# Optimization experiments

Hardware: AMD Instinct MI355X
Metric: run time of the kernel (lower is better)

## Reference

```python
import jax, jax.numpy as jnp
import numpy as np

B, T, D, H = 2, 2048, 1024, 16
HD = D // H
DFF = 4 * D
EPS = 1e-5


def gelu_tanh(x):
    c = jnp.sqrt(2.0 / jnp.pi).astype(x.dtype)
    return 0.5 * x * (1.0 + jnp.tanh(c * (x + 0.044715 * x ** 3)))


def layernorm(x, scale, shift):
    mean = jnp.mean(x, axis=-1, keepdims=True)
    var = jnp.var(x, axis=-1, keepdims=True)  # unbiased=False
    return (x - mean) / jnp.sqrt(var + EPS) * scale + shift


def setup_inputs() -> dict:
    key = jax.random.key(0)
    ks = jax.random.split(key, 12)
    s = lambda fan_in: 1.0 / np.sqrt(fan_in)
    return {
        "x": jax.random.normal(ks[0], (B, T, D), jnp.float32),
        "wq": jax.random.normal(ks[1], (D, D), jnp.float32) * s(D),
        "wk": jax.random.normal(ks[2], (D, D), jnp.float32) * s(D),
        "wv": jax.random.normal(ks[3], (D, D), jnp.float32) * s(D),
        "wo": jax.random.normal(ks[4], (D, D), jnp.float32) * s(D),
        "bo": jnp.zeros((D,), jnp.float32),
        "ln1_scale": jnp.ones((D,), jnp.float32),
        "ln1_shift": jnp.zeros((D,), jnp.float32),
        "ln2_scale": jnp.ones((D,), jnp.float32),
        "ln2_shift": jnp.zeros((D,), jnp.float32),
        "w1": jax.random.normal(ks[5], (D, DFF), jnp.float32) * s(D),
        "b1": jnp.zeros((DFF,), jnp.float32),
        "w2": jax.random.normal(ks[6], (DFF, D), jnp.float32) * s(DFF),
        "b2": jnp.zeros((D,), jnp.float32),
    }


def reference(x, wq, wk, wv, wo, bo, ln1_scale, ln1_shift, ln2_scale, ln2_shift, w1, b1, w2, b2):
    # pre-LN attention
    h = layernorm(x, ln1_scale, ln1_shift)
    q = (h @ wq).reshape(B, T, H, HD).transpose(0, 2, 1, 3)  # [B,H,T,hd]
    k = (h @ wk).reshape(B, T, H, HD).transpose(0, 2, 1, 3)
    v = (h @ wv).reshape(B, T, H, HD).transpose(0, 2, 1, 3)
    scores = jnp.einsum('bhqd,bhkd->bhqk', q, k) / jnp.sqrt(jnp.float32(HD))
    causal = jnp.tril(jnp.ones((T, T), bool))
    scores = jnp.where(causal, scores, -jnp.inf)
    attn = jax.nn.softmax(scores, axis=-1)
    ctx = jnp.einsum('bhqk,bhkd->bhqd', attn, v)
    ctx = ctx.transpose(0, 2, 1, 3).reshape(B, T, D)
    attn_out = ctx @ wo + bo
    x = x + attn_out  # dropout p=0
    # pre-LN FFN
    h2 = layernorm(x, ln2_scale, ln2_shift)
    ff = gelu_tanh(h2 @ w1 + b1) @ w2 + b2
    return x + ff
```

## Files before the change

### kernel.cpp

```cpp
#include <hip/hip_runtime.h>
#include <hip/hip_bf16.h>
#include <stdint.h>

typedef unsigned short u16;
typedef __attribute__((ext_vector_type(8))) short s16x8;
typedef __attribute__((ext_vector_type(4))) float f32x4;

#define B_   2
#define T_   2048
#define D_   1024
#define H_   16
#define HD_  64
#define DFF_ 4096
#define M_   (B_*T_)

#define SC2F 0.18033688f

__device__ __forceinline__ u16 f2b(float f){
  uint32_t u = __float_as_uint(f);
  u += 0x7FFFu + ((u >> 16) & 1u);
  return (u16)(u >> 16);
}
__device__ __forceinline__ float b2f(u16 u){ return __uint_as_float(((uint32_t)u) << 16); }
__device__ __forceinline__ uint32_t pk2(float lo, float hi){
  uint32_t r;
  asm volatile("v_cvt_pk_bf16_f32 %0, %1, %2" : "=v"(r) : "v"(lo), "v"(hi));
  return r;
}

__device__ __forceinline__ void gl_lds16(const void* g, void* l){
  __builtin_amdgcn_global_load_lds((const __attribute__((address_space(1))) void*)g,
                                   (__attribute__((address_space(3))) void*)l, 16, 0, 0);
}

template<int N> __device__ __forceinline__ void waitvm(){
  if constexpr (N == 0)      asm volatile("s_waitcnt vmcnt(0)" ::: "memory");
  else if constexpr (N == 2) asm volatile("s_waitcnt vmcnt(2)" ::: "memory");
  else                       asm volatile("s_waitcnt vmcnt(4)" ::: "memory");
}

__global__ __launch_bounds__(256) void wconv_all(const float* __restrict__ wq,
                                                 const float* __restrict__ wk,
                                                 const float* __restrict__ wv,
                                                 const float* __restrict__ wo,
                                                 const float* __restrict__ w1,
                                                 const float* __restrict__ w2,
                                                 u16* __restrict__ wqkvT, u16* __restrict__ woT,
                                                 u16* __restrict__ w1T,   u16* __restrict__ w2T,
                                                 const float* __restrict__ x,
                                                 const float* __restrict__ ln1s,
                                                 const float* __restrict__ ln1b,
                                                 u16* __restrict__ hout){
  const int bid = blockIdx.x;
  const int tid = threadIdx.x;
  if (bid >= 3072){
    const int row = bid - 3072;
    float4 a = reinterpret_cast<const float4*>(x + ((size_t)row << 10))[tid];
    float s = a.x + a.y + a.z + a.w;
    float q = a.x*a.x + a.y*a.y + a.z*a.z + a.w*a.w;
    #pragma unroll
    for (int o = 32; o > 0; o >>= 1){ s += __shfl_xor(s, o); q += __shfl_xor(q, o); }
    __shared__ float red[8];
    const int w = tid >> 6;
    if ((tid & 63) == 0){ red[w] = s; red[4 + w] = q; }
    __syncthreads();
    float S = red[0] + red[1] + red[2] + red[3];
    float Q = red[4] + red[5] + red[6] + red[7];
    float mean = S * (1.0f/1024.0f);
    float var  = Q * (1.0f/1024.0f) - mean*mean;
    float inv = rsqrtf(var + 1e-5f);
    float4 gsc = reinterpret_cast<const float4*>(ln1s)[tid];
    float4 gsh = reinterpret_cast<const float4*>(ln1b)[tid];
    ushort4 o4;
    o4.x = f2b((a.x - mean)*inv*gsc.x + gsh.x);
    o4.y = f2b((a.y - mean)*inv*gsc.y + gsh.y);
    o4.z = f2b((a.z - mean)*inv*gsc.z + gsh.z);
    o4.w = f2b((a.w - mean)*inv*gsc.w + gsh.w);
    reinterpret_cast<ushort4*>(hout + ((size_t)row << 10))[tid] = o4;
    return;
  }
  const float* W; u16* Wt; int K, N, tk, tn;
  if (bid < 1024){
    const int which = bid >> 8, t = bid & 255; tk = t >> 4; tn = t & 15; K = 1024; N = 1024;
    W  = (which == 0) ? wq : (which == 1) ? wk : (which == 2) ? wv : wo;
    Wt = (which == 3) ? woT : wqkvT + (size_t)which * D_ * D_;
  } else if (bid < 2048){
    const int t = bid - 1024; tk = t >> 6; tn = t & 63; K = 1024; N = 4096; W = w1; Wt = w1T;
  } else {
    const int t = bid - 2048; tk = t >> 4; tn = t & 15; K = 4096; N = 1024; W = w2; Wt = w2T;
  }
  const int k0 = tk << 6, n0 = tn << 6;
  __shared__ u16 tile[64][68];
  const int rr = tid >> 4, c4 = (tid & 15) << 2;
  #pragma unroll
  for (int rep = 0; rep < 4; rep++){
    int r = rr + (rep << 4);
    float4 v = *reinterpret_cast<const float4*>(W + (size_t)(k0 + r)*N + n0 + c4);
    tile[r][c4+0] = f2b(v.x); tile[r][c4+1] = f2b(v.y);
    tile[r][c4+2] = f2b(v.z); tile[r][c4+3] = f2b(v.w);
  }
  __syncthreads();
  const int rn = tid >> 2, kb = (tid & 3) << 4;
  u16 tmp[16];
  #pragma unroll
  for (int j = 0; j < 16; j++) tmp[j] = tile[kb + j][rn];
  ushort4* dst = reinterpret_cast<ushort4*>(Wt + (size_t)(n0 + rn)*K + k0 + kb);
  dst[0] = make_ushort4(tmp[0], tmp[1], tmp[2], tmp[3]);
  dst[1] = make_ushort4(tmp[4], tmp[5], tmp[6], tmp[7]);
  dst[2] = make_ushort4(tmp[8], tmp[9], tmp[10], tmp[11]);
  dst[3] = make_ushort4(tmp[12], tmp[13], tmp[14], tmp[15]);
}

__global__ __launch_bounds__(256) void vtrans(const u16* __restrict__ Vs, u16* __restrict__ Vt){
  const int bh = blockIdx.y, tt = blockIdx.x;
  __shared__ u16 tile[64][68];
  const int tid = threadIdx.x;
  const u16* src = Vs + ((size_t)bh*T_ + tt*64)*HD_;
  const int rr = tid >> 4, c4 = (tid & 15) << 2;
  #pragma unroll
  for (int rep = 0; rep < 4; rep++){
    int r = rr + (rep << 4);
    ushort4 v = *reinterpret_cast<const ushort4*>(src + (size_t)r*HD_ + c4);
    tile[r][c4+0] = v.x; tile[r][c4+1] = v.y; tile[r][c4+2] = v.z; tile[r][c4+3] = v.w;
  }
  __syncthreads();
  const int rn = tid >> 2, kb = (tid & 3) << 4;
  u16 tmp[16];
  #pragma unroll
  for (int j = 0; j < 16; j++) tmp[j] = tile[kb + j][rn];
  ushort4* dst = reinterpret_cast<ushort4*>(Vt + ((size_t)bh*HD_ + rn)*T_ + tt*64 + kb);
  dst[0] = make_ushort4(tmp[0], tmp[1], tmp[2], tmp[3]);
  dst[1] = make_ushort4(tmp[4], tmp[5], tmp[6], tmp[7]);
  dst[2] = make_ushort4(tmp[8], tmp[9], tmp[10], tmp[11]);
  dst[3] = make_ushort4(tmp[12], tmp[13], tmp[14], tmp[15]);
}

__global__ __launch_bounds__(256) void reduce2(const u16* __restrict__ p,
                                               const float* __restrict__ bias,
                                               const float* __restrict__ resid,
                                               float* __restrict__ out){
  const size_t idx = ((size_t)blockIdx.x << 8) + threadIdx.x;
  ushort4 a4 = reinterpret_cast<const ushort4*>(p)[idx];
  ushort4 b4 = reinterpret_cast<const ushort4*>(p)[idx + (((size_t)M_*D_) >> 2)];
  float4 r = reinterpret_cast<const float4*>(resid)[idx];
  float4 bb = reinterpret_cast<const float4*>(bias)[threadIdx.x];
  float4 o;
  o.x = b2f(a4.x) + b2f(b4.x) + r.x + bb.x;
  o.y = b2f(a4.y) + b2f(b4.y) + r.y + bb.y;
  o.z = b2f(a4.z) + b2f(b4.z) + r.z + bb.z;
  o.w = b2f(a4.w) + b2f(b4.w) + r.w + bb.w;
  reinterpret_cast<float4*>(out)[idx] = o;
}

__global__ __launch_bounds__(256) void reduce_ln(const u16* __restrict__ p,
                                                 const float* __restrict__ bias,
                                                 const float* __restrict__ resid,
                                                 const float* __restrict__ sc,
                                                 const float* __restrict__ sh,
                                                 float* __restrict__ x1,
                                                 u16* __restrict__ h2){
  const int row = blockIdx.x;
  const int tid = threadIdx.x;
  const size_t idx = ((size_t)row << 8) + tid;
  ushort4 a4 = reinterpret_cast<const ushort4*>(p)[idx];
  ushort4 b4 = reinterpret_cast<const ushort4*>(p)[idx + (((size_t)M_*D_) >> 2)];
  float4 r  = reinterpret_cast<const float4*>(resid)[idx];
  float4 bb = reinterpret_cast<const float4*>(bias)[tid];
  float4 v;
  v.x = b2f(a4.x) + b2f(b4.x) + r.x + bb.x;
  v.y = b2f(a4.y) + b2f(b4.y) + r.y + bb.y;
  v.z = b2f(a4.z) + b2f(b4.z) + r.z + bb.z;
  v.w = b2f(a4.w) + b2f(b4.w) + r.w + bb.w;
  reinterpret_cast<float4*>(x1)[idx] = v;
  float s = v.x + v.y + v.z + v.w;
  float q = v.x*v.x + v.y*v.y + v.z*v.z + v.w*v.w;
  #pragma unroll
  for (int o = 32; o > 0; o >>= 1){ s += __shfl_xor(s, o); q += __shfl_xor(q, o); }
  __shared__ float red[8];
  const int w = tid >> 6;
  if ((tid & 63) == 0){ red[w] = s; red[4 + w] = q; }
  __syncthreads();
  float S = red[0] + red[1] + red[2] + red[3];
  float Q = red[4] + red[5] + red[6] + red[7];
  float mean = S * (1.0f/1024.0f);
  float var  = Q * (1.0f/1024.0f) - mean*mean;
  float inv = rsqrtf(var + 1e-5f);
  float4 gsc = reinterpret_cast<const float4*>(sc)[tid];
  float4 gsh = reinterpret_cast<const float4*>(sh)[tid];
  ushort4 o4;
  o4.x = f2b((v.x - mean)*inv*gsc.x + gsh.x);
  o4.y = f2b((v.y - mean)*inv*gsc.y + gsh.y);
  o4.z = f2b((v.z - mean)*inv*gsc.z + gsh.z);
  o4.w = f2b((v.w - mean)*inv*gsc.w + gsh.w);
  reinterpret_cast<ushort4*>(h2 + ((size_t)row << 10))[tid] = o4;
}

template<int EPI, int NF>
__global__ __launch_bounds__(512, 2) void gemm8(const u16* __restrict__ A, const u16* __restrict__ Bt,
                                                const float* __restrict__ bias,
                                                void* __restrict__ Cv, int M, int N, int K, int lda){
  constexpr int BROWS = NF * 32;
  __shared__ __align__(16) u16 LA[2][2][128*64];
  __shared__ __align__(16) u16 LB[2][2][BROWS*64];
  const int tid = threadIdx.x;
  const int lane = tid & 63;
  const int w = tid >> 6;
  const int wm = w >> 2, wn = w & 3;
  const int g = lane >> 4, l15 = lane & 15;
  const int bnb = (wn & 1) * (NF * 16);

  const int nx = gridDim.x, ny = gridDim.y;
  const int nwg = nx * ny * gridDim.z;
  const int flat = blockIdx.x + nx * (blockIdx.y + ny * blockIdx.z);
  const int nfid = (flat & 7) * (nwg >> 3) + (flat >> 3);
  const int tn = nfid % nx;
  const int rest = nfid / nx;
  const int tm = rest % ny;
  const int kz = rest / ny;
  const int tn0 = tn * (NF * 64);
  const int tm0 = tm << 8;
  const u16* Az = A  + (size_t)kz * K;
  const u16* Bz = Bt + (size_t)kz * K;

  const int arow0 = tid >> 3,         asl0 = (((tid) & 7) ^ (arow0 & 7)) << 3;
  const int arow1 = (tid + 512) >> 3, asl1 = (((tid + 512) & 7) ^ (arow1 & 7)) << 3;

  f32x4 acc[8][NF];
  #pragma unroll
  for (int i = 0; i < 8; i++)
    #pragma unroll
    for (int j = 0; j < NF; j++) acc[i][j] = (f32x4){0.f,0.f,0.f,0.f};
  s16x8 bf[NF][2];

#define STG_A(db, h, tt) do{                                                        \
    gl_lds16(Az + (size_t)(tm0 + (h)*128 + arow0)*lda + ((tt) << 6) + asl0,         \
             &LA[db][h][tid*8]);                                                    \
    gl_lds16(Az + (size_t)(tm0 + (h)*128 + arow1)*lda + ((tt) << 6) + asl1,         \
             &LA[db][h][(tid + 512)*8]);                                            \
  }while(0)
#define STG_B(db, h, tt) do{                                                        \
    gl_lds16(Bz + (size_t)(tn0 + (h)*BROWS + arow0)*lda + ((tt) << 6) + asl0,       \
             &LB[db][h][tid*8]);                                                    \
    if constexpr (NF == 4){                                                         \
      gl_lds16(Bz + (size_t)(tn0 + (h)*BROWS + arow1)*lda + ((tt) << 6) + asl1,     \
               &LB[db][h][(tid + 512)*8]);                                          \
    }                                                                               \
  }while(0)
#define LDAF(db, mf, kk) (*reinterpret_cast<const s16x8*>(                          \
    &LA[db][wm][((mf)*16 + l15)*64 + ((((kk)*4 + g) ^ (l15 & 7)) << 3)]))
#define LDBF(db, nf, kk) (*reinterpret_cast<const s16x8*>(                          \
    &LB[db][wn >> 1][(bnb + (nf)*16 + l15)*64 + ((((kk)*4 + g) ^ (l15 & 7)) << 3)]))
#define BLOAD(db) do{ _Pragma("unroll")                                             \
    for (int nf = 0; nf < NF; nf++){ bf[nf][0] = LDBF(db, nf, 0);                   \
                                     bf[nf][1] = LDBF(db, nf, 1); } }while(0)
#define PH(db, MFA, MFB, STG, WV) do{                                               \
    s16x8 a00 = LDAF(db, MFA, 0), a01 = LDAF(db, MFA, 1);                           \
    s16x8 a10 = LDAF(db, MFB, 0), a11 = LDAF(db, MFB, 1);                           \
    STG;                                                                            \
    WV;                                                                             \
    __builtin_amdgcn_s_barrier();                                                   \
    __builtin_amdgcn_s_setprio(1);                                                  \
    _Pragma("unroll")                                                               \
    for (int nf = 0; nf < NF; nf++){                                                \
      acc[MFA][nf] = __builtin_amdgcn_mfma_f32_16x16x32_bf16(a00, bf[nf][0], acc[MFA][nf], 0,0,0); \
      acc[MFA][nf] = __builtin_amdgcn_mfma_f32_16x16x32_bf16(a01, bf[nf][1], acc[MFA][nf], 0,0,0); \
      acc[MFB][nf] = __builtin_amdgcn_mfma_f32_16x16x32_bf16(a10, bf[nf][0], acc[MFB][nf], 0,0,0); \
      acc[MFB][nf] = __builtin_amdgcn_mfma_f32_16x16x32_bf16(a11, bf[nf][1], acc[MFB][nf], 0,0,0); \
    }                                                                               \
    __builtin_amdgcn_s_setprio(0);                                                  \
    __builtin_amdgcn_s_barrier();                                                   \
  }while(0)

  const int NT = K >> 6;
  STG_B(0, 0, 0); STG_B(0, 1, 0); STG_A(0, 0, 0); STG_A(0, 1, 0);
  STG_B(1, 0, 1); STG_B(1, 1, 1);
  waitvm<NF>();
  __builtin_amdgcn_s_barrier();

  for (int t = 0; t < NT; t += 2){
    const bool last = (t + 2 >= NT);
    BLOAD(0);
    PH(0, 0, 1, STG_A(1, 0, t + 1), );
    PH(0, 2, 3, STG_A(1, 1, t + 1), );
    PH(0, 4, 5, if (!last) STG_B(0, 0, t + 2), );
    PH(0, 6, 7, if (!last) STG_B(0, 1, t + 2),
                if (last) waitvm<0>(); else waitvm<NF>(););
    BLOAD(1);
    PH(1, 0, 1, if (!last) STG_A(0, 0, t + 2), );
    PH(1, 2, 3, if (!last) STG_A(0, 1, t + 2), );
    PH(1, 4, 5, if (!last) STG_B(1, 0, t + 3), );
    PH(1, 6, 7, if (!last) STG_B(1, 1, t + 3),
                if (last) waitvm<0>(); else waitvm<NF>(););
  }
#undef STG_A
#undef STG_B
#undef LDAF
#undef LDBF
#undef BLOAD
#undef PH

  #pragma unroll
  for (int mf = 0; mf < 8; mf++){
    const int mb = tm0 + wm*128 + mf*16 + (g << 2);
    #pragma unroll
    for (int nf = 0; nf < NF; nf++){
      const int n = tn0 + wn*(NF*16) + nf*16 + l15;
      #pragma unroll
      for (int rr = 0; rr < 4; rr++){
        const int m = mb + rr;
        float v = acc[mf][nf][rr];
        if constexpr (EPI == 0){
          ((u16*)Cv)[(size_t)kz*((size_t)M*N) + (size_t)m*N + n] = f2b(v);
        } else if constexpr (EPI == 1){
          const int sel = n >> 10, nn = n & 1023;
          const int hh = nn >> 6, d = nn & 63;
          if (sel == 0) v *= SC2F;
          ((u16*)Cv)[(size_t)sel*((size_t)M_*D_) +
                     ((((size_t)(m >> 11)*H_ + hh)*T_ + (m & 2047)) << 6) + d] = f2b(v);
        } else {
          float u = v + bias[n];
          float t2 = 0.7978845608f*(u + 0.044715f*u*u*u);
          float e = __expf(2.0f*t2);
          float th = 1.0f - 2.0f/(e + 1.0f);
          ((u16*)Cv)[(size_t)m*N + n] = f2b(0.5f*u*(1.0f + th));
        }
      }
    }
  }
}

__global__ __launch_bounds__(512) void attn_k(const u16* __restrict__ Qg, const u16* __restrict__ Kg,
                                              const u16* __restrict__ Vg, u16* __restrict__ ctx){
  const int flat = blockIdx.x + (blockIdx.y << 4);
  const int xcd = flat & 7;
  const int j_  = (flat >> 3) & 31;
  const int half = flat >> 8;
  const int bh  = ((j_ & 3) << 3) + xcd;
  const int pr_ = j_ >> 2;
  const int qt  = half ? (15 - pr_) : pr_;
  const int NKT = (qt << 1) + 2;
  const int tid = threadIdx.x;
  const int lane = tid & 63;
  const int w = tid >> 6;
  const int g = lane >> 4, l15 = lane & 15;

  __shared__ __align__(16) u16 Qs[128*64];
  __shared__ __align__(16) u16 Ks[2][64*64];
  __shared__ __align__(16) u16 Vt[2][64*64];
  __shared__ __align__(16) u16 Pl[8][16*64];

  const size_t hb = (size_t)bh * ((size_t)T_*HD_);
  const u16* Qh = Qg + hb;
  const u16* Kh = Kg + hb;
  const u16* Vh = Vg + hb;
  const int b = bh >> 4, hh = bh & 15;

  const int s_r0 = tid >> 3,         s_c0 = (((tid & 7) ^ (s_r0 & 7)) << 3);
  const int s_r1 = (tid + 512) >> 3, s_c1 = ((((tid + 512) & 7) ^ (s_r1 & 7)) << 3);

  gl_lds16(Qh + (size_t)(qt*128 + s_r0)*HD_ + s_c0, Qs + tid*8);
  gl_lds16(Qh + (size_t)(qt*128 + s_r1)*HD_ + s_c1, Qs + (tid+512)*8);
  gl_lds16(Kh + (size_t)s_r0*HD_ + s_c0, Ks[0] + tid*8);
  gl_lds16(Vh + (size_t)s_r0*T_ + s_c0, Vt[0] + tid*8);
  __syncthreads();

  s16x8 qa[2];
  #pragma unroll
  for (int kk = 0; kk < 2; kk++){
    int ra = (w << 4) + l15;
    int slot = (kk << 2) + g;
    qa[kk] = *reinterpret_cast<const s16x8*>(Qs + ra*64 + ((slot ^ (ra & 7)) << 3));
  }

  f32x4 accO[4];
  #pragma unroll
  for (int j = 0; j < 4; j++) accO[j] = (f32x4){0.f,0.f,0.f,0.f};
  float mrow = -1e30f, lrow = 0.f;
  const int qgl = qt*128 + (w << 4) + l15;

  for (int kt = 0; kt < NKT; ++kt){
    const int cur = kt & 1, nxt = cur ^ 1;
    const bool pf = (kt + 1 < NKT);

    if (pf){
      gl_lds16(Kh + (size_t)((kt+1)*64 + s_r0)*HD_ + s_c0, Ks[nxt] + tid*8);
      gl_lds16(Vh + (size_t)s_r0*T_ + (kt+1)*64 + s_c0, Vt[nxt] + tid*8);
    }

    f32x4 accS[4];
    #pragma unroll
    for (int j = 0; j < 4; j++) accS[j] = (f32x4){0.f,0.f,0.f,0.f};
    __builtin_amdgcn_s_setprio(1);
    #pragma unroll
    for (int jn = 0; jn < 4; jn++){
      #pragma unroll
      for (int kk = 0; kk < 2; kk++){
        int rb = (jn << 4) + l15;
        int slot = (kk << 2) + g;
        s16x8 kf = *reinterpret_cast<const s16x8*>(Ks[cur] + rb*64 + ((slot ^ (rb & 7)) << 3));
        accS[jn] = __builtin_amdgcn_mfma_f32_16x16x32_bf16(kf, qa[kk], accS[jn], 0, 0, 0);
      }
    }
    __builtin_amdgcn_s_setprio(0);

    if (kt >= (qt << 1)){
      #pragma unroll
      for (int jn = 0; jn < 4; jn++)
        #pragma unroll
        for (int rr = 0; rr < 4; rr++){
          int kgl = kt*64 + (jn << 4) + (g << 2) + rr;
          if (kgl > qgl) accS[jn][rr] = -1e30f;
        }
    }

    float rmax = accS[0][0];
    #pragma unroll
    for (int jn = 0; jn < 4; jn++)
      #pragma unroll
      for (int rr = 0; rr < 4; rr++) rmax = fmaxf(rmax, accS[jn][rr]);
    rmax = fmaxf(rmax, __shfl_xor(rmax, 16));
    rmax = fmaxf(rmax, __shfl_xor(rmax, 32));

    if (__any(rmax > mrow + 8.0f)){
      float mn = fmaxf(mrow, rmax);
      float sf = exp2f(mrow - mn);
      mrow = mn;
      lrow *= sf;
      #pragma unroll
      for (int rr = 0; rr < 4; rr++){
        float sfr = __shfl(sf, ((lane >> 4) << 2) + rr);
        #pragma unroll
        for (int jn = 0; jn < 4; jn++) accO[jn][rr] *= sfr;
      }
    }

    float tsum = 0.f;
    #pragma unroll
    for (int jn = 0; jn < 4; jn++){
      float pv0 = exp2f(accS[jn][0] - mrow);
      float pv1 = exp2f(accS[jn][1] - mrow);
      float pv2 = exp2f(accS[jn][2] - mrow);
      float pv3 = exp2f(accS[jn][3] - mrow);
      tsum += (pv0 + pv1) + (pv2 + pv3);
      int slot = (jn << 1) | (g >> 1);
      int base = l15*64 + (((slot ^ (l15 & 7)) & 7) << 3) + ((g & 1) << 2);
      uint2 pkd = make_uint2(pk2(pv0, pv1), pk2(pv2, pv3));
      *reinterpret_cast<uint2*>(&Pl[w][base]) = pkd;
    }
    tsum += __shfl_xor(tsum, 16);
    tsum += __shfl_xor(tsum, 32);
    lrow += tsum;

    __builtin_amdgcn_s_setprio(1);
    #pragma unroll
    for (int kk = 0; kk < 2; kk++){
      int slot = (kk << 2) + g;
      s16x8 pa = *reinterpret_cast<const s16x8*>(
          &Pl[w][l15*64 + (((slot ^ (l15 & 7)) & 7) << 3)]);
      #pragma unroll
      for (int jn = 0; jn < 4; jn++){
        int vd = (jn << 4) + l15;
        s16x8 vbf = *reinterpret_cast<const s16x8*>(
            Vt[cur] + vd*64 + (((slot ^ (vd & 7)) & 7) << 3));
        accO[jn] = __builtin_amdgcn_mfma_f32_16x16x32_bf16(pa, vbf, accO[jn], 0, 0, 0);
      }
    }
    __builtin_amdgcn_s_setprio(0);

    __syncthreads();
  }

  #pragma unroll
  for (int rr = 0; rr < 4; rr++){
    float lr = __shfl(lrow, ((lane >> 4) << 2) + rr);
    float inv = 1.0f / lr;
    int qrow = qt*128 + (w << 4) + (g << 2) + rr;
    size_t rowbase = ((size_t)(b*T_ + qrow) << 10) + ((size_t)hh << 6);
    #pragma unroll
    for (int jn = 0; jn < 4; jn++){
      int d = (jn << 4) + l15;
      ctx[rowbase + d] = f2b(accO[jn][rr] * inv);
    }
  }
}

extern "C" void kernel_launch(void* const* d_in, const int* in_sizes, int n_in,
                              void* d_out, int out_size, void* d_ws, size_t ws_size,
                              hipStream_t stream){
  (void)in_sizes; (void)n_in; (void)out_size; (void)ws_size;
  const float* x    = (const float*)d_in[0];
  const float* wq   = (const float*)d_in[1];
  const float* wk   = (const float*)d_in[2];
  const float* wv   = (const float*)d_in[3];
  const float* wo   = (const float*)d_in[4];
  const float* bo   = (const float*)d_in[5];
  const float* ln1s = (const float*)d_in[6];
  const float* ln1b = (const float*)d_in[7];
  const float* ln2s = (const float*)d_in[8];
  const float* ln2b = (const float*)d_in[9];
  const float* w1   = (const float*)d_in[10];
  const float* b1   = (const float*)d_in[11];
  const float* w2   = (const float*)d_in[12];
  const float* b2   = (const float*)d_in[13];
  float* out = (float*)d_out;

  char* p = (char*)d_ws;
  u16*  wqkvT = (u16*)p;  p += (size_t)3*D_*D_*2;
  u16*  woT   = (u16*)p;  p += (size_t)D_*D_*2;
  u16*  w1T   = (u16*)p;  p += (size_t)D_*DFF_*2;
  u16*  w2T   = (u16*)p;  p += (size_t)DFF_*D_*2;
  u16*  h     = (u16*)p;  p += (size_t)M_*D_*2;
  u16*  qb    = (u16*)p;  p += (size_t)M_*D_*2;
  u16*  kb    = (u16*)p;  p += (size_t)M_*D_*2;
  u16*  vb    = (u16*)p;  p += (size_t)M_*D_*2;
  u16*  ctx   = (u16*)p;  p += (size_t)M_*D_*2;
  float* x1   = (float*)p; p += (size_t)M_*D_*4;
  u16*  h2    = (u16*)p;  p += (size_t)M_*D_*2;
  u16*  ff1   = (u16*)p;  p += (size_t)M_*DFF_*2;
  (void)kb;
  u16* part = h;

  dim3 blk(256), blk8(512);
  wconv_all<<<3072 + M_, blk, 0, stream>>>(wq, wk, wv, wo, w1, w2, wqkvT, woT, w1T, w2T,
                                           x, ln1s, ln1b, h);
  gemm8<1,4><<<dim3(12,16,1), blk8, 0, stream>>>(h, wqkvT, nullptr, qb, M_, 3*D_, D_, D_);
  vtrans<<<dim3(32,32), blk, 0, stream>>>(vb, h);
  attn_k<<<dim3(16,32), blk8, 0, stream>>>(qb, qb + (size_t)M_*D_, h, ctx);
  gemm8<0,2><<<dim3(8,16,2), blk8, 0, stream>>>(ctx, woT, nullptr, part, M_, D_, D_/2, D_);
  reduce_ln<<<M_, blk, 0, stream>>>(part, bo, x, ln2s, ln2b, x1, h2);
  gemm8<3,4><<<dim3(16,16,1), blk8, 0, stream>>>(h2, w1T, b1, ff1, M_, DFF_, D_, D_);
  gemm8<0,2><<<dim3(8,16,2), blk8, 0, stream>>>(ff1, w2T, nullptr, part, M_, D_, DFF_/2, DFF_);
  reduce2<<<M_, blk, 0, stream>>>(part, b2, x1, out);
}
```

Measured before the change: 231.4 us.

## Fuse V transpose into QKV GEMM epilogue and reuse Q smem for P

The QKV GEMM epilogue now writes the V block directly in transposed [b,h,d,t] layout through an LDS staging tile, so the separate vtrans kernel and its round trip through global memory are gone. The attention kernel drops its dedicated P buffer and reuses each wave's slice of the Q shared tile, which lowers LDS use and may allow higher occupancy. It also changes the block-to-(head, q-tile) mapping so adjacent blocks pair light and heavy causal tiles. The cost is extra syncs in the V-epilogue tiles, and the P-in-Q reuse is only safe if Q fragments are fully held in registers first.

Result: no change. 230.9 us (-0.2%).

```diff
diff --git a/kernel.cpp b/kernel.cpp
--- a/kernel.cpp
+++ b/kernel.cpp
@@ -105,30 +105,6 @@
   #pragma unroll
   for (int j = 0; j < 16; j++) tmp[j] = tile[kb + j][rn];
   ushort4* dst = reinterpret_cast<ushort4*>(Wt + (size_t)(n0 + rn)*K + k0 + kb);
-  dst[0] = make_ushort4(tmp[0], tmp[1], tmp[2], tmp[3]);
-  dst[1] = make_ushort4(tmp[4], tmp[5], tmp[6], tmp[7]);
-  dst[2] = make_ushort4(tmp[8], tmp[9], tmp[10], tmp[11]);
-  dst[3] = make_ushort4(tmp[12], tmp[13], tmp[14], tmp[15]);
-}
-
-__global__ __launch_bounds__(256) void vtrans(const u16* __restrict__ Vs, u16* __restrict__ Vt){
-  const int bh = blockIdx.y, tt = blockIdx.x;
-  __shared__ u16 tile[64][68];
-  const int tid = threadIdx.x;
-  const u16* src = Vs + ((size_t)bh*T_ + tt*64)*HD_;
-  const int rr = tid >> 4, c4 = (tid & 15) << 2;
-  #pragma unroll
-  for (int rep = 0; rep < 4; rep++){
-    int r = rr + (rep << 4);
-    ushort4 v = *reinterpret_cast<const ushort4*>(src + (size_t)r*HD_ + c4);
-    tile[r][c4+0] = v.x; tile[r][c4+1] = v.y; tile[r][c4+2] = v.z; tile[r][c4+3] = v.w;
-  }
-  __syncthreads();
-  const int rn = tid >> 2, kb = (tid & 3) << 4;
-  u16 tmp[16];
-  #pragma unroll
-  for (int j = 0; j < 16; j++) tmp[j] = tile[kb + j][rn];
-  ushort4* dst = reinterpret_cast<ushort4*>(Vt + ((size_t)bh*HD_ + rn)*T_ + tt*64 + kb);
   dst[0] = make_ushort4(tmp[0], tmp[1], tmp[2], tmp[3]);
   dst[1] = make_ushort4(tmp[4], tmp[5], tmp[6], tmp[7]);
   dst[2] = make_ushort4(tmp[8], tmp[9], tmp[10], tmp[11]);
@@ -198,7 +174,8 @@
 template<int EPI, int NF>
 __global__ __launch_bounds__(512, 2) void gemm8(const u16* __restrict__ A, const u16* __restrict__ Bt,
                                                 const float* __restrict__ bias,
-                                                void* __restrict__ Cv, int M, int N, int K, int lda){
+                                                void* __restrict__ Cv, void* __restrict__ Cv2,
+                                                int M, int N, int K, int lda){
   constexpr int BROWS = NF * 32;
   __shared__ __align__(16) u16 LA[2][2][128*64];
   __shared__ __align__(16) u16 LB[2][2][BROWS*64];
@@ -299,30 +276,86 @@
 #undef BLOAD
 #undef PH
 
-  #pragma unroll
-  for (int mf = 0; mf < 8; mf++){
-    const int mb = tm0 + wm*128 + mf*16 + (g << 2);
-    #pragma unroll
-    for (int nf = 0; nf < NF; nf++){
-      const int n = tn0 + wn*(NF*16) + nf*16 + l15;
-      #pragma unroll
-      for (int rr = 0; rr < 4; rr++){
-        const int m = mb + rr;
-        float v = acc[mf][nf][rr];
-        if constexpr (EPI == 0){
-          ((u16*)Cv)[(size_t)kz*((size_t)M*N) + (size_t)m*N + n] = f2b(v);
-        } else if constexpr (EPI == 1){
-          const int sel = n >> 10, nn = n & 1023;
+  if constexpr (EPI == 1){
+    const int sel = tn0 >> 10;
+    if (sel < 2){
+      #pragma unroll
+      for (int mf = 0; mf < 8; mf++){
+        const int mb = tm0 + wm*128 + mf*16 + (g << 2);
+        #pragma unroll
+        for (int nf = 0; nf < NF; nf++){
+          const int n = tn0 + wn*(NF*16) + nf*16 + l15;
+          const int nn = n & 1023;
           const int hh = nn >> 6, d = nn & 63;
-          if (sel == 0) v *= SC2F;
-          ((u16*)Cv)[(size_t)sel*((size_t)M_*D_) +
-                     ((((size_t)(m >> 11)*H_ + hh)*T_ + (m & 2047)) << 6) + d] = f2b(v);
-        } else {
-          float u = v + bias[n];
-          float t2 = 0.7978845608f*(u + 0.044715f*u*u*u);
-          float e = __expf(2.0f*t2);
-          float th = 1.0f - 2.0f/(e + 1.0f);
-          ((u16*)Cv)[(size_t)m*N + n] = f2b(0.5f*u*(1.0f + th));
+          #pragma unroll
+          for (int rr = 0; rr < 4; rr++){
+            const int m = mb + rr;
+            float v = acc[mf][nf][rr];
+            if (sel == 0) v *= SC2F;
+            ((u16*)Cv)[(size_t)sel*((size_t)M_*D_) +
+                       ((((size_t)(m >> 11)*H_ + hh)*T_ + (m & 2047)) << 6) + d] = f2b(v);
+          }
+        }
+      }
+    } else {
+      u16* TR = &LA[0][0][0];
+      u16* vt = (u16*)Cv2;
+      const int bq = tm0 >> 11;
+      const int tloc = tm0 & 2047;
+      #pragma unroll
+      for (int hp = 0; hp < 2; hp++){
+        __syncthreads();
+        if ((wn >> 1) == hp){
+          #pragma unroll
+          for (int mf = 0; mf < 8; mf++){
+            const int mb = wm*128 + mf*16 + (g << 2);
+            #pragma unroll
+            for (int nf = 0; nf < NF; nf++){
+              const int nr = ((wn & 1) << 6) + (nf << 4) + l15;
+              #pragma unroll
+              for (int rr = 0; rr < 4; rr++){
+                const int m = mb + rr;
+                TR[nr*256 + (((m >> 3) ^ (nr & 15)) << 3) + (m & 7)] = f2b(acc[mf][nf][rr]);
+              }
+            }
+          }
+        }
+        __syncthreads();
+        {
+          const int nr = tid >> 2;
+          const int m0 = (tid & 3) << 6;
+          const int nn = (tn0 & 1023) + (hp << 7) + nr;
+          const int hh = nn >> 6, d = nn & 63;
+          u16* dst = vt + (((size_t)(bq*H_ + hh))*HD_ + d)*T_ + tloc + m0;
+          #pragma unroll
+          for (int jj = 0; jj < 8; jj++){
+            const int j = (m0 >> 3) + jj;
+            s16x8 vv = *reinterpret_cast<const s16x8*>(&TR[nr*256 + ((j ^ (nr & 15)) << 3)]);
+            *reinterpret_cast<s16x8*>(dst + jj*8) = vv;
+          }
+        }
+      }
+    }
+  } else {
+    #pragma unroll
+    for (int mf = 0; mf < 8; mf++){
+      const int mb = tm0 + wm*128 + mf*16 + (g << 2);
+      #pragma unroll
+      for (int nf = 0; nf < NF; nf++){
+        const int n = tn0 + wn*(NF*16) + nf*16 + l15;
+        #pragma unroll
+        for (int rr = 0; rr < 4; rr++){
+          const int m = mb + rr;
+          float v = acc[mf][nf][rr];
+          if constexpr (EPI == 0){
+            ((u16*)Cv)[(size_t)kz*((size_t)M*N) + (size_t)m*N + n] = f2b(v);
+          } else {
+            float u = v + bias[n];
+            float t2 = 0.7978845608f*(u + 0.044715f*u*u*u);
+            float e = __expf(2.0f*t2);
+            float th = 1.0f - 2.0f/(e + 1.0f);
+            ((u16*)Cv)[(size_t)m*N + n] = f2b(0.5f*u*(1.0f + th));
+          }
         }
       }
     }
@@ -333,11 +366,11 @@
                                               const u16* __restrict__ Vg, u16* __restrict__ ctx){
   const int flat = blockIdx.x + (blockIdx.y << 4);
   const int xcd = flat & 7;
-  const int j_  = (flat >> 3) & 31;
-  const int half = flat >> 8;
-  const int bh  = ((j_ & 3) << 3) + xcd;
-  const int pr_ = j_ >> 2;
-  const int qt  = half ? (15 - pr_) : pr_;
+  const int idx = flat >> 3;
+  const int pair_ = idx >> 1, parity = idx & 1;
+  const int bh  = ((pair_ & 3) << 3) + xcd;
+  const int pr_ = pair_ >> 2;
+  const int qt  = parity ? (15 - pr_) : pr_;
   const int NKT = (qt << 1) + 2;
   const int tid = threadIdx.x;
   const int lane = tid & 63;
@@ -347,7 +380,7 @@
   __shared__ __align__(16) u16 Qs[128*64];
   __shared__ __align__(16) u16 Ks[2][64*64];
   __shared__ __align__(16) u16 Vt[2][64*64];
-  __shared__ __align__(16) u16 Pl[8][16*64];
+  u16* const Plw = Qs + (w << 10);
 
   const size_t hb = (size_t)bh * ((size_t)T_*HD_);
   const u16* Qh = Qg + hb;
@@ -445,7 +478,7 @@
       int slot = (jn << 1) | (g >> 1);
       int base = l15*64 + (((slot ^ (l15 & 7)) & 7) << 3) + ((g & 1) << 2);
       uint2 pkd = make_uint2(pk2(pv0, pv1), pk2(pv2, pv3));
-      *reinterpret_cast<uint2*>(&Pl[w][base]) = pkd;
+      *reinterpret_cast<uint2*>(&Plw[base]) = pkd;
     }
     tsum += __shfl_xor(tsum, 16);
     tsum += __shfl_xor(tsum, 32);
@@ -456,7 +489,7 @@
     for (int kk = 0; kk < 2; kk++){
       int slot = (kk << 2) + g;
       s16x8 pa = *reinterpret_cast<const s16x8*>(
-          &Pl[w][l15*64 + (((slot ^ (l15 & 7)) & 7) << 3)]);
+          &Plw[l15*64 + (((slot ^ (l15 & 7)) & 7) << 3)]);
       #pragma unroll
       for (int jn = 0; jn < 4; jn++){
         int vd = (jn << 4) + l15;
@@ -517,18 +550,17 @@
   float* x1   = (float*)p; p += (size_t)M_*D_*4;
   u16*  h2    = (u16*)p;  p += (size_t)M_*D_*2;
   u16*  ff1   = (u16*)p;  p += (size_t)M_*DFF_*2;
-  (void)kb;
+  (void)kb; (void)vb;
   u16* part = h;
 
   dim3 blk(256), blk8(512);
   wconv_all<<<3072 + M_, blk, 0, stream>>>(wq, wk, wv, wo, w1, w2, wqkvT, woT, w1T, w2T,
                                            x, ln1s, ln1b, h);
-  gemm8<1,4><<<dim3(12,16,1), blk8, 0, stream>>>(h, wqkvT, nullptr, qb, M_, 3*D_, D_, D_);
-  vtrans<<<dim3(32,32), blk, 0, stream>>>(vb, h);
-  attn_k<<<dim3(16,32), blk8, 0, stream>>>(qb, qb + (size_t)M_*D_, h, ctx);
-  gemm8<0,2><<<dim3(8,16,2), blk8, 0, stream>>>(ctx, woT, nullptr, part, M_, D_, D_/2, D_);
+  gemm8<1,4><<<dim3(12,16,1), blk8, 0, stream>>>(h, wqkvT, nullptr, qb, ff1, M_, 3*D_, D_, D_);
+  attn_k<<<dim3(16,32), blk8, 0, stream>>>(qb, qb + (size_t)M_*D_, ff1, ctx);
+  gemm8<0,2><<<dim3(8,16,2), blk8, 0, stream>>>(ctx, woT, nullptr, part, nullptr, M_, D_, D_/2, D_);
   reduce_ln<<<M_, blk, 0, stream>>>(part, bo, x, ln2s, ln2b, x1, h2);
-  gemm8<3,4><<<dim3(16,16,1), blk8, 0, stream>>>(h2, w1T, b1, ff1, M_, DFF_, D_, D_);
-  gemm8<0,2><<<dim3(8,16,2), blk8, 0, stream>>>(ff1, w2T, nullptr, part, M_, D_, DFF_/2, DFF_);
+  gemm8<3,4><<<dim3(16,16,1), blk8, 0, stream>>>(h2, w1T, b1, ff1, nullptr, M_, DFF_, D_, D_);
+  gemm8<0,2><<<dim3(8,16,2), blk8, 0, stream>>>(ff1, w2T, nullptr, part, nullptr, M_, D_, DFF_/2, DFF_);
   reduce2<<<M_, blk, 0, stream>>>(part, b2, x1, out);
 }
```
